# Kernel optimization log

Hardware: AMD Instinct MI355X
Metric: run time of the kernel (lower is better)

Reference implementation:

```python
import jax, jax.numpy as jnp
import numpy as np

B, N, F = 2, 512, 128
NUM_BASIS = 4


def _mlp(x, W1, b1, W2, b2, W3, b3):
    # two hidden ReLU layers, linear output -> [..., NUM_BASIS]
    h = jax.nn.relu(x @ W1 + b1)
    h = jax.nn.relu(h @ W2 + b2)
    return h @ W3 + b3


def setup_inputs() -> dict:
    key = jax.random.key(0)
    ks = jax.random.split(key, 12)
    s = 0.05  # keep activations O(1)
    inp = {
        "pointwise_features": jax.random.normal(ks[0], (B, N, F), jnp.float32),
        "relative_features": jax.random.normal(ks[1], (B, N, N, F), jnp.float32),
        "pointwise_basis": jax.random.normal(ks[2], (B, N, NUM_BASIS, 3), jnp.float32),
        "relative_basis": jax.random.normal(ks[3], (B, N, N, NUM_BASIS, 3), jnp.float32),
        "pw_W1": jax.random.normal(ks[4], (F, 128), jnp.float32) * s,
        "pw_b1": jnp.zeros((128,), jnp.float32),
        "pw_W2": jax.random.normal(ks[5], (128, 128), jnp.float32) * s,
        "pw_b2": jnp.zeros((128,), jnp.float32),
        "pw_W3": jax.random.normal(ks[6], (128, NUM_BASIS), jnp.float32) * s,
        "pw_b3": jnp.zeros((NUM_BASIS,), jnp.float32),
        "rel_W1": jax.random.normal(ks[7], (F, 128), jnp.float32) * s,
        "rel_b1": jnp.zeros((128,), jnp.float32),
        "rel_W2": jax.random.normal(ks[8], (128, 128), jnp.float32) * s,
        "rel_b2": jnp.zeros((128,), jnp.float32),
        "rel_W3": jax.random.normal(ks[9], (128, NUM_BASIS), jnp.float32) * s,
        "rel_b3": jnp.zeros((NUM_BASIS,), jnp.float32),
        # last 64 atoms are padding (masked) in every batch element
        "masked_elements": jnp.broadcast_to(jnp.arange(N) >= N - 64, (B, N)),
    }
    return inp


def reference(pointwise_features, relative_features, pointwise_basis, relative_basis,
              pw_W1, pw_b1, pw_W2, pw_b2, pw_W3, pw_b3,
              rel_W1, rel_b1, rel_W2, rel_b2, rel_W3, rel_b3,
              masked_elements):
    unmasked = ~masked_elements                      # [B, N]
    num_atoms = unmasked.sum(-1).astype(pointwise_features.dtype)  # [B]

    # pointwise_shift: [B, N, K, 3]
    pw_scale = _mlp(pointwise_features, pw_W1, pw_b1, pw_W2, pw_b2, pw_W3, pw_b3)
    pointwise_shift = pointwise_basis * pw_scale[..., None]

    # relative_shift: [B, N, N, K, 3], mask over j, mean over j
    rel_scale = _mlp(relative_features, rel_W1, rel_b1, rel_W2, rel_b2, rel_W3, rel_b3)
    relative_shift = relative_basis * rel_scale[..., None]
    relative_shift = relative_shift * unmasked[:, None, :, None, None]
    relative_shift = relative_shift.sum(-3) / num_atoms[:, None, None, None]  # [B, N, K, 3]

    all_shifts = pointwise_shift + relative_shift
    shift = all_shifts.sum(-2) / num_atoms[:, None, None]  # [B, N, 3]
    return shift
```

## Files before the change

kernel.cpp:

```cpp
#include <hip/hip_runtime.h>
#include <stdint.h>

#define LDK 136

typedef __attribute__((ext_vector_type(4))) float f32x4;
typedef __attribute__((ext_vector_type(8))) short bf16x8;

__device__ inline unsigned short f2bf_rtne(float f) {
    union { float f; unsigned u; } v; v.f = f;
    unsigned u = v.u;
    u += 0x7fffu + ((u >> 16) & 1u);
    return (unsigned short)(u >> 16);
}

__global__ void prep_kernel(const float* __restrict__ relW1, const float* __restrict__ relW2,
                            const float* __restrict__ pwW1, const float* __restrict__ pwW2,
                            const float* __restrict__ relW3, const float* __restrict__ pwW3,
                            const void* __restrict__ maskp,
                            float* __restrict__ maskf, float* __restrict__ na,
                            unsigned short* __restrict__ w1T_rel, unsigned short* __restrict__ w2T_rel,
                            unsigned short* __restrict__ w1T_pw, unsigned short* __restrict__ w2T_pw,
                            unsigned short* __restrict__ w3T_rel, unsigned short* __restrict__ w3T_pw) {
    int t = threadIdx.x;
    const float* srcs[4] = {relW1, relW2, pwW1, pwW2};
    unsigned short* dsts[4] = {w1T_rel, w2T_rel, w1T_pw, w2T_pw};
    int e0 = blockIdx.x * 1024 + t;
#pragma unroll
    for (int i = 0; i < 4; ++i) {
        int e = e0 + i * 256;
        int mat = e >> 14, o = e & 16383;
        int n = o >> 7, k = o & 127;
        dsts[mat][o] = f2bf_rtne(srcs[mat][k * 128 + n]);
    }
    if (blockIdx.x == 1) {
        for (int i = t; i < 2048; i += 256) {
            int r = i >> 7, h = i & 127;
            w3T_rel[i] = (r < 4) ? f2bf_rtne(relW3[h * 4 + r]) : (unsigned short)0;
            w3T_pw[i]  = (r < 4) ? f2bf_rtne(pwW3[h * 4 + r])  : (unsigned short)0;
        }
    }
    if (blockIdx.x == 0) {
        __shared__ int anyb;
        __shared__ float cnt[2];
        if (t == 0) anyb = 0;
        if (t < 2) cnt[t] = 0.f;
        __syncthreads();
        const unsigned char* mb = (const unsigned char*)maskp;
        int la = 0;
        for (int i = t; i < 1024; i += 256) la |= mb[i];
        if (la) atomicOr(&anyb, 1);
        __syncthreads();
        bool isbyte = (anyb != 0);
        const int* mi = (const int*)maskp;
        float loc0 = 0.f, loc1 = 0.f;
        for (int i = t; i < 1024; i += 256) {
            int v = isbyte ? (int)mb[i] : mi[i];
            float um = (v != 0) ? 0.f : 1.f;
            maskf[i] = um;
            if (i < 512) loc0 += um; else loc1 += um;
        }
        atomicAdd(&cnt[0], loc0);
        atomicAdd(&cnt[1], loc1);
        __syncthreads();
        if (t < 2) na[t] = cnt[t];
    }
}

__global__ __launch_bounds__(256, 2)
void mlp_kernel(const float* __restrict__ X,
                const unsigned short* __restrict__ w1T,
                const unsigned short* __restrict__ w2T,
                const unsigned short* __restrict__ w3T,
                const float* __restrict__ b1, const float* __restrict__ b2,
                const float* __restrict__ b3,
                float* __restrict__ Sout) {
    __shared__ short xs[64 * LDK];
    __shared__ short hs[2][64 * LDK];
    __shared__ float bs1[128], bs2[128], b3s[4];

    int t = threadIdx.x;
    int w = t >> 6, lane = t & 63, q = lane >> 4, col = lane & 15;

    if (t < 128) { bs1[t] = b1[t]; bs2[t] = b2[t]; }
    if (t < 4) b3s[t] = b3[t];

    bf16x8 w1f[2][4], w2f[2][4], w3f[4];
#pragma unroll
    for (int tn = 0; tn < 2; ++tn)
#pragma unroll
        for (int kc = 0; kc < 4; ++kc) {
            int n = w * 32 + tn * 16 + col;
            int kk = kc * 32 + q * 8;
            w1f[tn][kc] = *(const bf16x8*)&w1T[n * 128 + kk];
            w2f[tn][kc] = *(const bf16x8*)&w2T[n * 128 + kk];
        }
#pragma unroll
    for (int kc = 0; kc < 4; ++kc)
        w3f[kc] = *(const bf16x8*)&w3T[col * 128 + kc * 32 + q * 8];

    long rowbase = (long)blockIdx.x * 256;
    int r0 = t >> 5, cg = t & 31;

    float4 px[8];
    {
        const float4* Xg = (const float4*)(X + rowbase * 128);
#pragma unroll
        for (int i = 0; i < 8; ++i) px[i] = Xg[(r0 + 8 * i) * 32 + cg];
#pragma unroll
        for (int i = 0; i < 8; ++i) {
            float4 v = px[i];
            short4 s4 = make_short4((short)f2bf_rtne(v.x), (short)f2bf_rtne(v.y),
                                    (short)f2bf_rtne(v.z), (short)f2bf_rtne(v.w));
            *(short4*)&xs[(r0 + 8 * i) * LDK + cg * 4] = s4;
        }
    }
    __syncthreads();

    for (int tile = 0; tile < 4; ++tile) {
        int hp = tile & 1;
        if (tile < 3) {
            const float4* Xg2 = (const float4*)(X + (rowbase + (long)(tile + 1) * 64) * 128);
#pragma unroll
            for (int i = 0; i < 8; ++i) px[i] = Xg2[(r0 + 8 * i) * 32 + cg];
        }

        f32x4 acc[2][4];
#pragma unroll
        for (int tn = 0; tn < 2; ++tn)
#pragma unroll
            for (int tm = 0; tm < 4; ++tm) acc[tn][tm] = (f32x4)(0.f);
#pragma unroll
        for (int kc = 0; kc < 4; ++kc) {
            bf16x8 bf[4];
#pragma unroll
            for (int tm = 0; tm < 4; ++tm)
                bf[tm] = *(const bf16x8*)&xs[(tm * 16 + col) * LDK + kc * 32 + q * 8];
#pragma unroll
            for (int tn = 0; tn < 2; ++tn)
#pragma unroll
                for (int tm = 0; tm < 4; ++tm)
                    acc[tn][tm] = __builtin_amdgcn_mfma_f32_16x16x32_bf16(w1f[tn][kc], bf[tm], acc[tn][tm], 0, 0, 0);
        }

#pragma unroll
        for (int tn = 0; tn < 2; ++tn)
#pragma unroll
            for (int tm = 0; tm < 4; ++tm) {
                int n0 = w * 32 + tn * 16 + q * 4;
                int m = tm * 16 + col;
                float4 bb = *(const float4*)&bs1[n0];
                short4 s4 = make_short4(
                    (short)f2bf_rtne(fmaxf(acc[tn][tm][0] + bb.x, 0.f)),
                    (short)f2bf_rtne(fmaxf(acc[tn][tm][1] + bb.y, 0.f)),
                    (short)f2bf_rtne(fmaxf(acc[tn][tm][2] + bb.z, 0.f)),
                    (short)f2bf_rtne(fmaxf(acc[tn][tm][3] + bb.w, 0.f)));
                *(short4*)&hs[hp][m * LDK + n0] = s4;
            }
        __syncthreads();

        if (tile < 3) {
#pragma unroll
            for (int i = 0; i < 8; ++i) {
                float4 v = px[i];
                short4 s4 = make_short4((short)f2bf_rtne(v.x), (short)f2bf_rtne(v.y),
                                        (short)f2bf_rtne(v.z), (short)f2bf_rtne(v.w));
                *(short4*)&xs[(r0 + 8 * i) * LDK + cg * 4] = s4;
            }
        }

        f32x4 acc2[2][4];
#pragma unroll
        for (int tn = 0; tn < 2; ++tn)
#pragma unroll
            for (int tm = 0; tm < 4; ++tm) acc2[tn][tm] = (f32x4)(0.f);
#pragma unroll
        for (int kc = 0; kc < 4; ++kc) {
            bf16x8 bf[4];
#pragma unroll
            for (int tm = 0; tm < 4; ++tm)
                bf[tm] = *(const bf16x8*)&hs[hp][(tm * 16 + col) * LDK + kc * 32 + q * 8];
#pragma unroll
            for (int tn = 0; tn < 2; ++tn)
#pragma unroll
                for (int tm = 0; tm < 4; ++tm)
                    acc2[tn][tm] = __builtin_amdgcn_mfma_f32_16x16x32_bf16(w2f[tn][kc], bf[tm], acc2[tn][tm], 0, 0, 0);
        }
        __syncthreads();

#pragma unroll
        for (int tn = 0; tn < 2; ++tn)
#pragma unroll
            for (int tm = 0; tm < 4; ++tm) {
                int n0 = w * 32 + tn * 16 + q * 4;
                int m = tm * 16 + col;
                float4 bb = *(const float4*)&bs2[n0];
                short4 s4 = make_short4(
                    (short)f2bf_rtne(fmaxf(acc2[tn][tm][0] + bb.x, 0.f)),
                    (short)f2bf_rtne(fmaxf(acc2[tn][tm][1] + bb.y, 0.f)),
                    (short)f2bf_rtne(fmaxf(acc2[tn][tm][2] + bb.z, 0.f)),
                    (short)f2bf_rtne(fmaxf(acc2[tn][tm][3] + bb.w, 0.f)));
                *(short4*)&hs[hp][m * LDK + n0] = s4;
            }
        __syncthreads();

        {
            f32x4 a3 = (f32x4)(0.f);
#pragma unroll
            for (int kc = 0; kc < 4; ++kc) {
                bf16x8 hb = *(const bf16x8*)&hs[hp][(w * 16 + col) * LDK + kc * 32 + q * 8];
                a3 = __builtin_amdgcn_mfma_f32_16x16x32_bf16(w3f[kc], hb, a3, 0, 0, 0);
            }
            if (q == 0) {
                long r = rowbase + (long)tile * 64 + w * 16 + col;
                *(float4*)&Sout[r * 4] = make_float4(a3[0] + b3s[0], a3[1] + b3s[1],
                                                     a3[2] + b3s[2], a3[3] + b3s[3]);
            }
        }
    }
}

__global__ __launch_bounds__(256)
void reduce_kernel(const float* __restrict__ S_rel, const float* __restrict__ S_pw,
                   const float* __restrict__ rel_basis, const float* __restrict__ pw_basis,
                   const float* __restrict__ maskf, const float* __restrict__ na,
                   float* __restrict__ out) {
    int bi = blockIdx.x;
    int b = bi >> 9;
    int t = threadIdx.x;
    float part[12];
#pragma unroll
    for (int r = 0; r < 12; ++r) part[r] = 0.f;

    for (int j = t; j < 512; j += 256) {
        float m = maskf[b * 512 + j];
        long r = (long)bi * 512 + j;
        float4 s4 = *(const float4*)&S_rel[r * 4];
        const float* bp = &rel_basis[r * 12];
        float4 q0 = *(const float4*)&bp[0];
        float4 q1 = *(const float4*)&bp[4];
        float4 q2 = *(const float4*)&bp[8];
        float s0 = s4.x * m, s1 = s4.y * m, s2 = s4.z * m, s3 = s4.w * m;
        part[0] += s0 * q0.x; part[1] += s0 * q0.y; part[2]  += s0 * q0.z;
        part[3] += s1 * q0.w; part[4] += s1 * q1.x; part[5]  += s1 * q1.y;
        part[6] += s2 * q1.z; part[7] += s2 * q1.w; part[8]  += s2 * q2.x;
        part[9] += s3 * q2.y; part[10] += s3 * q2.z; part[11] += s3 * q2.w;
    }

#pragma unroll
    for (int s = 32; s > 0; s >>= 1)
#pragma unroll
        for (int r = 0; r < 12; ++r) part[r] += __shfl_down(part[r], s);

    __shared__ float red[4][12];
    int w = t >> 6, lane = t & 63;
    if (lane == 0)
#pragma unroll
        for (int r = 0; r < 12; ++r) red[w][r] = part[r];
    __syncthreads();

    if (t < 3) {
        float NA = na[b];
        float accp = 0.f, rel = 0.f;
#pragma unroll
        for (int k = 0; k < 4; ++k) {
            rel  += red[0][k * 3 + t] + red[1][k * 3 + t] + red[2][k * 3 + t] + red[3][k * 3 + t];
            accp += pw_basis[bi * 12 + k * 3 + t] * S_pw[bi * 4 + k];
        }
        out[bi * 3 + t] = accp / NA + rel / (NA * NA);
    }
}

extern "C" void kernel_launch(void* const* d_in, const int* in_sizes, int n_in,
                              void* d_out, int out_size, void* d_ws, size_t ws_size,
                              hipStream_t stream) {
    const float* pw_feat   = (const float*)d_in[0];
    const float* rel_feat  = (const float*)d_in[1];
    const float* pw_basis  = (const float*)d_in[2];
    const float* rel_basis = (const float*)d_in[3];
    const float* pw_W1 = (const float*)d_in[4];
    const float* pw_b1 = (const float*)d_in[5];
    const float* pw_W2 = (const float*)d_in[6];
    const float* pw_b2 = (const float*)d_in[7];
    const float* pw_W3 = (const float*)d_in[8];
    const float* pw_b3 = (const float*)d_in[9];
    const float* rel_W1 = (const float*)d_in[10];
    const float* rel_b1 = (const float*)d_in[11];
    const float* rel_W2 = (const float*)d_in[12];
    const float* rel_b2 = (const float*)d_in[13];
    const float* rel_W3 = (const float*)d_in[14];
    const float* rel_b3 = (const float*)d_in[15];
    const void*  maskp  = d_in[16];
    float* out = (float*)d_out;

    char* ws = (char*)d_ws;
    float* maskf = (float*)(ws + 0);
    float* na    = (float*)(ws + 4096);
    unsigned short* w1T_rel = (unsigned short*)(ws + 4352);
    unsigned short* w2T_rel = (unsigned short*)(ws + 37120);
    unsigned short* w1T_pw  = (unsigned short*)(ws + 69888);
    unsigned short* w2T_pw  = (unsigned short*)(ws + 102656);
    unsigned short* w3T_rel = (unsigned short*)(ws + 135424);
    unsigned short* w3T_pw  = (unsigned short*)(ws + 139520);
    float* S_pw  = (float*)(ws + 143616);
    float* S_rel = (float*)(ws + 160000);

    prep_kernel<<<64, 256, 0, stream>>>(rel_W1, rel_W2, pw_W1, pw_W2, rel_W3, pw_W3, maskp,
                                        maskf, na, w1T_rel, w2T_rel, w1T_pw, w2T_pw,
                                        w3T_rel, w3T_pw);
    mlp_kernel<<<2048, 256, 0, stream>>>(rel_feat, w1T_rel, w2T_rel, w3T_rel,
                                         rel_b1, rel_b2, rel_b3, S_rel);
    mlp_kernel<<<4, 256, 0, stream>>>(pw_feat, w1T_pw, w2T_pw, w3T_pw,
                                      pw_b1, pw_b2, pw_b3, S_pw);
    reduce_kernel<<<1024, 256, 0, stream>>>(S_rel, S_pw, rel_basis, pw_basis,
                                            maskf, na, out);
}
```

Baseline: 444.1 us.

## Fuse basis reduction into MLP kernel and skip fully masked row tiles

```diff
diff --git a/kernel.cpp b/kernel.cpp
--- a/kernel.cpp
+++ b/kernel.cpp
@@ -18,6 +18,7 @@
                             const float* __restrict__ relW3, const float* __restrict__ pwW3,
                             const void* __restrict__ maskp,
                             float* __restrict__ maskf, float* __restrict__ na,
+                            int* __restrict__ gflag, float* __restrict__ out,
                             unsigned short* __restrict__ w1T_rel, unsigned short* __restrict__ w2T_rel,
                             unsigned short* __restrict__ w1T_pw, unsigned short* __restrict__ w2T_pw,
                             unsigned short* __restrict__ w3T_rel, unsigned short* __restrict__ w3T_pw) {
@@ -38,6 +39,9 @@
             w3T_rel[i] = (r < 4) ? f2bf_rtne(relW3[h * 4 + r]) : (unsigned short)0;
             w3T_pw[i]  = (r < 4) ? f2bf_rtne(pwW3[h * 4 + r])  : (unsigned short)0;
         }
+    }
+    if (blockIdx.x == 2) {
+        for (int i = t; i < 3072; i += 256) out[i] = 0.f;
     }
     if (blockIdx.x == 0) {
         __shared__ int anyb;
@@ -63,26 +67,62 @@
         atomicAdd(&cnt[1], loc1);
         __syncthreads();
         if (t < 2) na[t] = cnt[t];
+        if (t < 16) {
+            float s = 0.f;
+            for (int j = 0; j < 64; ++j) s += maskf[t * 64 + j];
+            gflag[t] = (s > 0.f) ? 1 : 0;
+        }
     }
 }
 
 __global__ __launch_bounds__(256, 2)
-void mlp_kernel(const float* __restrict__ X,
-                const unsigned short* __restrict__ w1T,
-                const unsigned short* __restrict__ w2T,
-                const unsigned short* __restrict__ w3T,
-                const float* __restrict__ b1, const float* __restrict__ b2,
-                const float* __restrict__ b3,
-                float* __restrict__ Sout) {
+void mlp_kernel(const float* __restrict__ Xrel, const float* __restrict__ Xpw,
+                const unsigned short* __restrict__ w1Tr, const unsigned short* __restrict__ w2Tr,
+                const unsigned short* __restrict__ w3Tr,
+                const unsigned short* __restrict__ w1Tp, const unsigned short* __restrict__ w2Tp,
+                const unsigned short* __restrict__ w3Tp,
+                const float* __restrict__ b1r, const float* __restrict__ b2r, const float* __restrict__ b3r,
+                const float* __restrict__ b1p, const float* __restrict__ b2p, const float* __restrict__ b3p,
+                const float* __restrict__ rel_basis, const float* __restrict__ pw_basis,
+                const float* __restrict__ maskf, const float* __restrict__ na,
+                const int* __restrict__ gflag,
+                float* __restrict__ out) {
     __shared__ short xs[64 * LDK];
-    __shared__ short hs[2][64 * LDK];
+    __shared__ short hs[64 * LDK];
     __shared__ float bs1[128], bs2[128], b3s[4];
+    __shared__ float Sl[256];
+    __shared__ float red[4][4][3];
 
     int t = threadIdx.x;
     int w = t >> 6, lane = t & 63, q = lane >> 4, col = lane & 15;
 
+    bool isrel = (blockIdx.x >= 4);
+    int rb = isrel ? ((int)blockIdx.x - 4) : (int)blockIdx.x;
+
+    const float* X = isrel ? Xrel : Xpw;
+    const unsigned short* w1T = isrel ? w1Tr : w1Tp;
+    const unsigned short* w2T = isrel ? w2Tr : w2Tp;
+    const unsigned short* w3T = isrel ? w3Tr : w3Tp;
+    const float* b1 = isrel ? b1r : b1p;
+    const float* b2 = isrel ? b2r : b2p;
+    const float* b3 = isrel ? b3r : b3p;
+
     if (t < 128) { bs1[t] = b1[t]; bs2[t] = b2[t]; }
     if (t < 4) b3s[t] = b3[t];
+
+    int b = isrel ? (rb >> 10) : (rb >> 1);
+    float NA = na[b];
+    float scale = isrel ? (1.f / (NA * NA)) : (1.f / NA);
+
+    int apack = 0x3210, nact = 4;
+    if (isrel) {
+        apack = 0; nact = 0;
+        int gbase = b * 8 + (rb & 1) * 4;
+#pragma unroll
+        for (int tt = 0; tt < 4; ++tt)
+            if (gflag[gbase + tt]) { apack |= tt << (4 * nact); ++nact; }
+        if (nact == 0) return;
+    }
 
     bf16x8 w1f[2][4], w2f[2][4], w3f[4];
 #pragma unroll
@@ -98,12 +138,13 @@
     for (int kc = 0; kc < 4; ++kc)
         w3f[kc] = *(const bf16x8*)&w3T[col * 128 + kc * 32 + q * 8];
 
-    long rowbase = (long)blockIdx.x * 256;
+    long rowbase = (long)rb * 256;
     int r0 = t >> 5, cg = t & 31;
+    int arow = t >> 2, ak = t & 3;
 
     float4 px[8];
     {
-        const float4* Xg = (const float4*)(X + rowbase * 128);
+        const float4* Xg = (const float4*)(X + (rowbase + (long)(apack & 15) * 64) * 128);
 #pragma unroll
         for (int i = 0; i < 8; ++i) px[i] = Xg[(r0 + 8 * i) * 32 + cg];
 #pragma unroll
@@ -116,12 +157,24 @@
     }
     __syncthreads();
 
-    for (int tile = 0; tile < 4; ++tile) {
-        int hp = tile & 1;
-        if (tile < 3) {
-            const float4* Xg2 = (const float4*)(X + (rowbase + (long)(tile + 1) * 64) * 128);
+    float p0 = 0.f, p1 = 0.f, p2 = 0.f;
+
+    for (int a = 0; a < nact; ++a) {
+        int tile = (apack >> (4 * a)) & 15;
+        long trow = rowbase + (long)tile * 64;
+
+        if (a + 1 < nact) {
+            int tnx = (apack >> (4 * (a + 1))) & 15;
+            const float4* Xg2 = (const float4*)(X + (rowbase + (long)tnx * 64) * 128);
 #pragma unroll
             for (int i = 0; i < 8; ++i) px[i] = Xg2[(r0 + 8 * i) * 32 + cg];
+        }
+
+        float bas0 = 0.f, bas1 = 0.f, bas2 = 0.f, mrow = 0.f;
+        if (isrel) {
+            const float* bp = &rel_basis[(trow + arow) * 12 + ak * 3];
+            bas0 = bp[0]; bas1 = bp[1]; bas2 = bp[2];
+            mrow = maskf[b * 512 + (rb & 1) * 256 + tile * 64 + w * 16 + col];
         }
 
         f32x4 acc[2][4];
@@ -154,11 +207,11 @@
                     (short)f2bf_rtne(fmaxf(acc[tn][tm][1] + bb.y, 0.f)),
                     (short)f2bf_rtne(fmaxf(acc[tn][tm][2] + bb.z, 0.f)),
                     (short)f2bf_rtne(fmaxf(acc[tn][tm][3] + bb.w, 0.f)));
-                *(short4*)&hs[hp][m * LDK + n0] = s4;
-            }
-        __syncthreads();
-
-        if (tile < 3) {
+                *(short4*)&hs[m * LDK + n0] = s4;
+            }
+        __syncthreads();
+
+        if (a + 1 < nact) {
 #pragma unroll
             for (int i = 0; i < 8; ++i) {
                 float4 v = px[i];
@@ -178,7 +231,7 @@
             bf16x8 bf[4];
 #pragma unroll
             for (int tm = 0; tm < 4; ++tm)
-                bf[tm] = *(const bf16x8*)&hs[hp][(tm * 16 + col) * LDK + kc * 32 + q * 8];
+                bf[tm] = *(const bf16x8*)&hs[(tm * 16 + col) * LDK + kc * 32 + q * 8];
 #pragma unroll
             for (int tn = 0; tn < 2; ++tn)
 #pragma unroll
@@ -199,7 +252,7 @@
                     (short)f2bf_rtne(fmaxf(acc2[tn][tm][1] + bb.y, 0.f)),
                     (short)f2bf_rtne(fmaxf(acc2[tn][tm][2] + bb.z, 0.f)),
                     (short)f2bf_rtne(fmaxf(acc2[tn][tm][3] + bb.w, 0.f)));
-                *(short4*)&hs[hp][m * LDK + n0] = s4;
+                *(short4*)&hs[m * LDK + n0] = s4;
             }
         __syncthreads();
 
@@ -207,66 +260,53 @@
             f32x4 a3 = (f32x4)(0.f);
 #pragma unroll
             for (int kc = 0; kc < 4; ++kc) {
-                bf16x8 hb = *(const bf16x8*)&hs[hp][(w * 16 + col) * LDK + kc * 32 + q * 8];
+                bf16x8 hb = *(const bf16x8*)&hs[(w * 16 + col) * LDK + kc * 32 + q * 8];
                 a3 = __builtin_amdgcn_mfma_f32_16x16x32_bf16(w3f[kc], hb, a3, 0, 0, 0);
             }
-            if (q == 0) {
-                long r = rowbase + (long)tile * 64 + w * 16 + col;
-                *(float4*)&Sout[r * 4] = make_float4(a3[0] + b3s[0], a3[1] + b3s[1],
-                                                     a3[2] + b3s[2], a3[3] + b3s[3]);
-            }
-        }
-    }
-}
-
-__global__ __launch_bounds__(256)
-void reduce_kernel(const float* __restrict__ S_rel, const float* __restrict__ S_pw,
-                   const float* __restrict__ rel_basis, const float* __restrict__ pw_basis,
-                   const float* __restrict__ maskf, const float* __restrict__ na,
-                   float* __restrict__ out) {
-    int bi = blockIdx.x;
-    int b = bi >> 9;
-    int t = threadIdx.x;
-    float part[12];
-#pragma unroll
-    for (int r = 0; r < 12; ++r) part[r] = 0.f;
-
-    for (int j = t; j < 512; j += 256) {
-        float m = maskf[b * 512 + j];
-        long r = (long)bi * 512 + j;
-        float4 s4 = *(const float4*)&S_rel[r * 4];
-        const float* bp = &rel_basis[r * 12];
-        float4 q0 = *(const float4*)&bp[0];
-        float4 q1 = *(const float4*)&bp[4];
-        float4 q2 = *(const float4*)&bp[8];
-        float s0 = s4.x * m, s1 = s4.y * m, s2 = s4.z * m, s3 = s4.w * m;
-        part[0] += s0 * q0.x; part[1] += s0 * q0.y; part[2]  += s0 * q0.z;
-        part[3] += s1 * q0.w; part[4] += s1 * q1.x; part[5]  += s1 * q1.y;
-        part[6] += s2 * q1.z; part[7] += s2 * q1.w; part[8]  += s2 * q2.x;
-        part[9] += s3 * q2.y; part[10] += s3 * q2.z; part[11] += s3 * q2.w;
-    }
-
-#pragma unroll
-    for (int s = 32; s > 0; s >>= 1)
-#pragma unroll
-        for (int r = 0; r < 12; ++r) part[r] += __shfl_down(part[r], s);
-
-    __shared__ float red[4][12];
-    int w = t >> 6, lane = t & 63;
-    if (lane == 0)
-#pragma unroll
-        for (int r = 0; r < 12; ++r) red[w][r] = part[r];
-    __syncthreads();
-
-    if (t < 3) {
-        float NA = na[b];
-        float accp = 0.f, rel = 0.f;
-#pragma unroll
-        for (int k = 0; k < 4; ++k) {
-            rel  += red[0][k * 3 + t] + red[1][k * 3 + t] + red[2][k * 3 + t] + red[3][k * 3 + t];
-            accp += pw_basis[bi * 12 + k * 3 + t] * S_pw[bi * 4 + k];
-        }
-        out[bi * 3 + t] = accp / NA + rel / (NA * NA);
+            if (isrel) {
+                if (q == 0) {
+                    float4 sm = make_float4((a3[0] + b3s[0]) * mrow, (a3[1] + b3s[1]) * mrow,
+                                            (a3[2] + b3s[2]) * mrow, (a3[3] + b3s[3]) * mrow);
+                    *(float4*)&Sl[(w * 16 + col) * 4] = sm;
+                }
+            } else if (q == 0) {
+                long bi = trow + w * 16 + col;
+                float s0 = a3[0] + b3s[0], s1 = a3[1] + b3s[1];
+                float s2 = a3[2] + b3s[2], s3 = a3[3] + b3s[3];
+                const float* pbp = &pw_basis[bi * 12];
+                float o0 = s0 * pbp[0] + s1 * pbp[3] + s2 * pbp[6] + s3 * pbp[9];
+                float o1 = s0 * pbp[1] + s1 * pbp[4] + s2 * pbp[7] + s3 * pbp[10];
+                float o2 = s0 * pbp[2] + s1 * pbp[5] + s2 * pbp[8] + s3 * pbp[11];
+                atomicAdd(&out[bi * 3 + 0], o0 * scale);
+                atomicAdd(&out[bi * 3 + 1], o1 * scale);
+                atomicAdd(&out[bi * 3 + 2], o2 * scale);
+            }
+        }
+        __syncthreads();
+
+        if (isrel) {
+            float sk = Sl[arow * 4 + ak];
+            p0 += sk * bas0; p1 += sk * bas1; p2 += sk * bas2;
+        }
+    }
+
+    if (isrel) {
+#pragma unroll
+        for (int s = 32; s >= 4; s >>= 1) {
+            p0 += __shfl_down(p0, s);
+            p1 += __shfl_down(p1, s);
+            p2 += __shfl_down(p2, s);
+        }
+        if (lane < 4) { red[w][lane][0] = p0; red[w][lane][1] = p1; red[w][lane][2] = p2; }
+        __syncthreads();
+        if (t < 3) {
+            float v = 0.f;
+#pragma unroll
+            for (int ww = 0; ww < 4; ++ww)
+#pragma unroll
+                for (int k = 0; k < 4; ++k) v += red[ww][k][t];
+            atomicAdd(&out[(long)(rb >> 1) * 3 + t], v * scale);
+        }
     }
 }
 
@@ -295,22 +335,22 @@
     char* ws = (char*)d_ws;
     float* maskf = (float*)(ws + 0);
     float* na    = (float*)(ws + 4096);
+    int*   gflag = (int*)(ws + 4160);
     unsigned short* w1T_rel = (unsigned short*)(ws + 4352);
     unsigned short* w2T_rel = (unsigned short*)(ws + 37120);
     unsigned short* w1T_pw  = (unsigned short*)(ws + 69888);
     unsigned short* w2T_pw  = (unsigned short*)(ws + 102656);
     unsigned short* w3T_rel = (unsigned short*)(ws + 135424);
     unsigned short* w3T_pw  = (unsigned short*)(ws + 139520);
-    float* S_pw  = (float*)(ws + 143616);
-    float* S_rel = (float*)(ws + 160000);
 
     prep_kernel<<<64, 256, 0, stream>>>(rel_W1, rel_W2, pw_W1, pw_W2, rel_W3, pw_W3, maskp,
-                                        maskf, na, w1T_rel, w2T_rel, w1T_pw, w2T_pw,
+                                        maskf, na, gflag, out,
+                                        w1T_rel, w2T_rel, w1T_pw, w2T_pw,
                                         w3T_rel, w3T_pw);
-    mlp_kernel<<<2048, 256, 0, stream>>>(rel_feat, w1T_rel, w2T_rel, w3T_rel,
-                                         rel_b1, rel_b2, rel_b3, S_rel);
-    mlp_kernel<<<4, 256, 0, stream>>>(pw_feat, w1T_pw, w2T_pw, w3T_pw,
-                                      pw_b1, pw_b2, pw_b3, S_pw);
-    reduce_kernel<<<1024, 256, 0, stream>>>(S_rel, S_pw, rel_basis, pw_basis,
-                                            maskf, na, out);
+    mlp_kernel<<<2052, 256, 0, stream>>>(rel_feat, pw_feat,
+                                         w1T_rel, w2T_rel, w3T_rel,
+                                         w1T_pw, w2T_pw, w3T_pw,
+                                         rel_b1, rel_b2, rel_b3,
+                                         pw_b1, pw_b2, pw_b3,
+                                         rel_basis, pw_basis, maskf, na, gflag, out);
 }
```

After: 421.7 us. 1.05x faster.
